# Optimization experiments

Hardware: AMD Instinct MI355X
Metric: run time of the kernel (lower is better)

Reference implementation:

```python
import jax, jax.numpy as jnp
import numpy as np

K = 2  # max_diffusion_step
UNITS = 128
NUM_NODES = 1024


def _diffusion_conv(x, support, W, b):
    # x: (B, N, D) ; Chebyshev diffusion over scaled Laplacian support (N, N)
    x0 = x
    x1 = jnp.einsum('nm,bmd->bnd', support, x0)
    xs = [x0, x1]
    for _ in range(K - 1):
        xs.append(2.0 * jnp.einsum('nm,bmd->bnd', support, xs[-1]) - xs[-2])
    feats = jnp.concatenate(xs, axis=-1)  # (B, N, D*(K+1))
    return feats @ W + b


def _gclstm_cell(x, h, c, support, W, b):
    gates = _diffusion_conv(jnp.concatenate([x, h], axis=-1), support, W, b)
    i, f, o, g = jnp.split(gates, 4, axis=-1)
    c_new = jax.nn.sigmoid(f) * c + jax.nn.sigmoid(i) * jnp.tanh(g)
    h_new = jax.nn.sigmoid(o) * jnp.tanh(c_new)
    return h_new, c_new


def setup_inputs() -> dict:
    key = jax.random.key(0)
    ks = jax.random.split(key, 8)
    B, S, N, H = 64, 12, NUM_NODES, UNITS

    # build scaled-Laplacian support from a sparse random symmetric adjacency
    rng = np.random.default_rng(0)
    A = (rng.random((N, N)) < 0.01).astype(np.float32)
    A = np.maximum(A, A.T)
    np.fill_diagonal(A, 0.0)
    d = A.sum(axis=1)
    d_is = 1.0 / np.sqrt(np.maximum(d, 1.0))
    L = np.eye(N, dtype=np.float32) - (d_is[:, None] * A * d_is[None, :])
    support = (L - np.eye(N, dtype=np.float32)).astype(np.float32)  # lambda_max ~ 2

    def lin(k, shape, fan_in):
        return jax.random.normal(k, shape, jnp.float32) / np.sqrt(fan_in)

    return {
        'inputs': jax.random.normal(ks[0], (B, N, 1), jnp.float32),
        'encoder_outputs': jax.random.normal(ks[1], (S, B, N, H), jnp.float32),
        'hidden_state': jax.random.normal(ks[2], (2, B, N, H), jnp.float32),
        'cell_state': jax.random.normal(ks[3], (2, B, N, H), jnp.float32),
        'supports': jnp.asarray(support),
        'w0': lin(ks[4], ((1 + H) * (K + 1), 4 * H), (1 + H) * (K + 1)),
        'b0': jnp.zeros((4 * H,), jnp.float32),
        'w1': lin(ks[5], ((H + H) * (K + 1), 4 * H), 2 * H * (K + 1)),
        'b1': jnp.zeros((4 * H,), jnp.float32),
        'attn_w': lin(ks[6], (H, H), H),
        'attn_b': jnp.zeros((H,), jnp.float32),
        'proj_w': lin(ks[7], (2 * H, 1), 2 * H),
        'proj_b': jnp.zeros((1,), jnp.float32),
    }


def reference(inputs, encoder_outputs, hidden_state, cell_state, supports,
              w0, b0, w1, b1, attn_w, attn_b, proj_w, proj_b):
    out = inputs
    hs, cs = [], []
    for layer, (W, b) in enumerate([(w0, b0), (w1, b1)]):
        h_new, c_new = _gclstm_cell(out, hidden_state[layer], cell_state[layer],
                                    supports, W, b)
        hs.append(h_new)
        cs.append(c_new)
        out = h_new  # (B, N, H)

    # additive attention: energy (S,B,N) -> softmax over S
    energy = jnp.tanh(encoder_outputs @ attn_w + attn_b)          # (S,B,N,H)
    energy = jnp.sum(energy * out[None], axis=-1)                 # (S,B,N)
    attention_weights = jax.nn.softmax(jnp.transpose(energy, (1, 2, 0)), axis=-1)  # (B,N,S)

    # bmm context gather
    context = jnp.einsum('bns,sbnh->bnh', attention_weights, encoder_outputs)

    cat = jnp.concatenate([out, context], axis=-1)                # (B,N,2H)
    projected = cat @ proj_w + proj_b                             # (B,N,out_dim)
    B = out.shape[0]
    output = projected.reshape(B, -1)                             # (B, N*out_dim)
    return output, jnp.stack(hs), jnp.stack(cs), attention_weights
```

## Files before the change

kernel.cpp:

```cpp
#include <hip/hip_runtime.h>
#include <hip/hip_bf16.h>
#include <stdint.h>

#define NB 64
#define NN 1024
#define NH 128
#define NS 12
#define BN (NB*NN)
#define D0 129
#define K0P 416
#define K1 768
#define NG 512
#define MAXNNZ 128
#define CH 16384
#define NCHUNK (BN/CH)

typedef __hip_bfloat16 bf16;
typedef float v4f __attribute__((ext_vector_type(4)));
typedef __bf16 v8bf __attribute__((ext_vector_type(8)));

__device__ __forceinline__ float bf2f(bf16 x) { return __bfloat162float(x); }
__device__ __forceinline__ bf16 f2bf(float x) { return __float2bfloat16(x); }
__device__ __forceinline__ float sane(float x) { return __builtin_isfinite(x) ? x : 0.f; }

__device__ __forceinline__ float loadF(const void* p, size_t i, int f32) {
  return f32 ? ((const float*)p)[i] : bf2f(((const bf16*)p)[i]);
}
__device__ __forceinline__ void storeF(void* p, size_t i, float v, int f32) {
  if (f32) ((float*)p)[i] = v; else ((bf16*)p)[i] = f2bf(v);
}
__device__ __forceinline__ v8bf load8(const void* p, size_t i, int f32) {
  v8bf r;
  if (f32) {
    const float* fp = (const float*)p + i;
#pragma unroll
    for (int j = 0; j < 8; ++j) r[j] = (__bf16)fp[j];
  } else {
    r = *(const v8bf*)((const bf16*)p + i);
  }
  return r;
}

__global__ void detect_dtype(const unsigned short* __restrict__ probe, int* __restrict__ flag) {
  int t = threadIdx.x;
  unsigned short x = probe[2 * t];
  int e = (x >> 7) & 0xFF;
  int insane = !((x & 0x7FFF) == 0 || (e >= 117 && e <= 131));
  __shared__ int cnt;
  if (t == 0) cnt = 0;
  __syncthreads();
  atomicAdd(&cnt, insane);
  __syncthreads();
  if (t == 0) *flag = (cnt > 64) ? 1 : 0;
}

__global__ void build_csr(const void* __restrict__ sup, int* __restrict__ cols,
                          float* __restrict__ vals, int* __restrict__ cnt,
                          const int* __restrict__ flag) {
  int f32 = *flag;
  int n = blockIdx.x;
  __shared__ int cn;
  if (threadIdx.x == 0) cn = 0;
  __syncthreads();
  for (int m = threadIdx.x; m < NN; m += blockDim.x) {
    float v = loadF(sup, (size_t)n * NN + m, f32);
    if (v != 0.0f && __builtin_isfinite(v)) {
      int slot = atomicAdd(&cn, 1);
      if (slot < MAXNNZ) { cols[n * MAXNNZ + slot] = m; vals[n * MAXNNZ + slot] = v; }
    }
  }
  __syncthreads();
  if (threadIdx.x == 0) cnt[n] = (cn < MAXNNZ) ? cn : MAXNNZ;
}

__global__ void pack_wt(const void* __restrict__ w, bf16* __restrict__ bt,
                        int K, int Kp, int Nn, const int* __restrict__ flag) {
  int f32 = *flag;
  int n = blockIdx.x;
  for (int k = threadIdx.x; k < Kp; k += blockDim.x) {
    float v = (k < K) ? loadF(w, (size_t)k * Nn + n, f32) : 0.0f;
    bt[(size_t)n * Kp + k] = f2bf(v);
  }
}

__global__ void diffuse0_a(const void* __restrict__ xin, const void* __restrict__ h0,
                           const int* __restrict__ cols, const float* __restrict__ vals,
                           const int* __restrict__ cnt, bf16* __restrict__ feats,
                           const int* __restrict__ flag, int R) {
  int f32 = *flag;
  int bn = R + blockIdx.x;
  int lbn = blockIdx.x;
  int n = bn & (NN - 1);
  int b = bn >> 10;
  int d = threadIdx.x;
  bf16* frow = feats + (size_t)lbn * K0P;
  if (d < D0) {
    float x0 = (d == 0) ? loadF(xin, bn, f32) : loadF(h0, (size_t)bn * NH + d - 1, f32);
    frow[d] = f2bf(x0);
    float acc = 0.f;
    int c = cnt[n];
    for (int j = 0; j < c; ++j) {
      int m = cols[n * MAXNNZ + j];
      float s = vals[n * MAXNNZ + j];
      int bm = (b << 10) | m;
      float xv = (d == 0) ? loadF(xin, bm, f32) : loadF(h0, (size_t)bm * NH + d - 1, f32);
      acc += s * xv;
    }
    frow[D0 + d] = f2bf(acc);
  } else if (d < D0 + (K0P - 3 * D0)) {
    frow[3 * D0 + (d - D0)] = f2bf(0.f);
  }
}

__global__ void diffuse0_b(const void* __restrict__ xin, const void* __restrict__ h0,
                           const int* __restrict__ cols, const float* __restrict__ vals,
                           const int* __restrict__ cnt, bf16* __restrict__ feats,
                           const int* __restrict__ flag, int R) {
  int f32 = *flag;
  int bn = R + blockIdx.x;
  int lbn = blockIdx.x;
  int n = bn & (NN - 1);
  int b = bn >> 10;
  int d = threadIdx.x;
  if (d >= D0) return;
  float x0 = (d == 0) ? loadF(xin, bn, f32) : loadF(h0, (size_t)bn * NH + d - 1, f32);
  float acc = -x0;
  int c = cnt[n];
  for (int j = 0; j < c; ++j) {
    int m = cols[n * MAXNNZ + j];
    float s = vals[n * MAXNNZ + j];
    int lbm = ((b << 10) | m) - R;
    float x1 = bf2f(feats[(size_t)lbm * K0P + D0 + d]);
    acc += 2.f * s * x1;
  }
  feats[(size_t)lbn * K0P + 2 * D0 + d] = f2bf(acc);
}

__global__ void diffuse1_a(const void* __restrict__ dout, size_t offH0,
                           const void* __restrict__ hidden, size_t offH1in,
                           const int* __restrict__ cols, const float* __restrict__ vals,
                           const int* __restrict__ cnt, bf16* __restrict__ feats,
                           const int* __restrict__ flag, int R) {
  int f32 = *flag;
  int bn = R + blockIdx.x;
  int lbn = blockIdx.x;
  int n = bn & (NN - 1);
  int b = bn >> 10;
  int d = threadIdx.x;
  bf16* frow = feats + (size_t)lbn * K1;
  float x0 = (d < NH) ? loadF(dout, offH0 + (size_t)bn * NH + d, f32)
                      : loadF(hidden, offH1in + (size_t)bn * NH + d - NH, f32);
  frow[d] = f2bf(x0);
  float acc = 0.f;
  int c = cnt[n];
  for (int j = 0; j < c; ++j) {
    int m = cols[n * MAXNNZ + j];
    float s = vals[n * MAXNNZ + j];
    size_t bm = (size_t)((b << 10) | m) * NH;
    float xv = (d < NH) ? loadF(dout, offH0 + bm + d, f32)
                        : loadF(hidden, offH1in + bm + d - NH, f32);
    acc += s * xv;
  }
  frow[256 + d] = f2bf(acc);
}

__global__ void diffuse1_b(const void* __restrict__ dout, size_t offH0,
                           const void* __restrict__ hidden, size_t offH1in,
                           const int* __restrict__ cols, const float* __restrict__ vals,
                           const int* __restrict__ cnt, bf16* __restrict__ feats,
                           const int* __restrict__ flag, int R) {
  int f32 = *flag;
  int bn = R + blockIdx.x;
  int lbn = blockIdx.x;
  int n = bn & (NN - 1);
  int b = bn >> 10;
  int d = threadIdx.x;
  float x0 = (d < NH) ? loadF(dout, offH0 + (size_t)bn * NH + d, f32)
                      : loadF(hidden, offH1in + (size_t)bn * NH + d - NH, f32);
  float acc = -x0;
  int c = cnt[n];
  for (int j = 0; j < c; ++j) {
    int m = cols[n * MAXNNZ + j];
    float s = vals[n * MAXNNZ + j];
    int lbm = ((b << 10) | m) - R;
    float x1 = bf2f(feats[(size_t)lbm * K1 + 256 + d]);
    acc += 2.f * s * x1;
  }
  feats[(size_t)lbn * K1 + 512 + d] = f2bf(acc);
}

__global__ __launch_bounds__(256) void gemm_bt(const bf16* __restrict__ A,
    const bf16* __restrict__ Bt, const void* __restrict__ bias,
    bf16* __restrict__ C, int Kd, const int* __restrict__ flag) {
  int f32 = *flag;
  __shared__ __align__(16) unsigned short As[128 * 32];
  __shared__ __align__(16) unsigned short Bs[128 * 32];
  const int tid = threadIdx.x;
  const int l = tid & 63;
  const int w = tid >> 6;
  const int wm = w >> 1, wn = w & 1;
  const int m0 = blockIdx.x * 128;
  const int n0 = blockIdx.y * 128;
  const bf16* Ab = A + (size_t)m0 * Kd;
  const bf16* Bb = Bt + (size_t)n0 * Kd;
  const int lr = l & 15, q = l >> 4;
  v4f acc[4][4] = {};
  for (int k0 = 0; k0 < Kd; k0 += 32) {
    v8bf ga[2], gb[2];
#pragma unroll
    for (int t = 0; t < 2; ++t) {
      int s = tid + 256 * t;
      int row = s >> 2, col = (s & 3) * 8;
      ga[t] = *(const v8bf*)(Ab + (size_t)row * Kd + k0 + col);
      gb[t] = *(const v8bf*)(Bb + (size_t)row * Kd + k0 + col);
    }
    __syncthreads();
#pragma unroll
    for (int t = 0; t < 2; ++t) {
      int s = tid + 256 * t;
      int row = s >> 2, col = (s & 3) * 8;
      *(v8bf*)&As[row * 32 + col] = ga[t];
      *(v8bf*)&Bs[row * 32 + col] = gb[t];
    }
    __syncthreads();
    v8bf af[4], bfv[4];
#pragma unroll
    for (int i = 0; i < 4; ++i) {
      af[i]  = *(const v8bf*)&As[(wm * 64 + i * 16 + lr) * 32 + q * 8];
      bfv[i] = *(const v8bf*)&Bs[(wn * 64 + i * 16 + lr) * 32 + q * 8];
    }
#pragma unroll
    for (int mt = 0; mt < 4; ++mt)
#pragma unroll
      for (int nt = 0; nt < 4; ++nt)
        acc[mt][nt] = __builtin_amdgcn_mfma_f32_16x16x32_bf16(af[mt], bfv[nt], acc[mt][nt], 0, 0, 0);
    __syncthreads();
  }
#pragma unroll
  for (int nt = 0; nt < 4; ++nt) {
    int n = n0 + wn * 64 + nt * 16 + lr;
    float bv = loadF(bias, n, f32);
#pragma unroll
    for (int mt = 0; mt < 4; ++mt)
#pragma unroll
      for (int r = 0; r < 4; ++r) {
        int m = m0 + wm * 64 + mt * 16 + q * 4 + r;
        C[(size_t)m * NG + n] = f2bf(acc[mt][nt][r] + bv);
      }
  }
}

__global__ __launch_bounds__(256) void gemm_energy(const void* __restrict__ enc,
    const bf16* __restrict__ Bt, const void* __restrict__ bias,
    const void* __restrict__ dout, size_t offH1, float* __restrict__ energy,
    const int* __restrict__ flag) {
  int f32 = *flag;
  __shared__ __align__(16) unsigned short As[128 * 32];
  __shared__ __align__(16) unsigned short Bs[128 * 32];
  const int tid = threadIdx.x;
  const int l = tid & 63;
  const int w = tid >> 6;
  const int wm = w >> 1, wn = w & 1;
  const int m0 = blockIdx.x * 128;
  const int lr = l & 15, q = l >> 4;
  v4f acc[4][4] = {};
  for (int k0 = 0; k0 < NH; k0 += 32) {
    v8bf ga[2], gb[2];
#pragma unroll
    for (int t = 0; t < 2; ++t) {
      int s = tid + 256 * t;
      int row = s >> 2, col = (s & 3) * 8;
      ga[t] = load8(enc, (size_t)(m0 + row) * NH + k0 + col, f32);
      gb[t] = *(const v8bf*)(Bt + (size_t)row * NH + k0 + col);
    }
    __syncthreads();
#pragma unroll
    for (int t = 0; t < 2; ++t) {
      int s = tid + 256 * t;
      int row = s >> 2, col = (s & 3) * 8;
      *(v8bf*)&As[row * 32 + col] = ga[t];
      *(v8bf*)&Bs[row * 32 + col] = gb[t];
    }
    __syncthreads();
    v8bf af[4], bfv[4];
#pragma unroll
    for (int i = 0; i < 4; ++i) {
      af[i]  = *(const v8bf*)&As[(wm * 64 + i * 16 + lr) * 32 + q * 8];
      bfv[i] = *(const v8bf*)&Bs[(wn * 64 + i * 16 + lr) * 32 + q * 8];
    }
#pragma unroll
    for (int mt = 0; mt < 4; ++mt)
#pragma unroll
      for (int nt = 0; nt < 4; ++nt)
        acc[mt][nt] = __builtin_amdgcn_mfma_f32_16x16x32_bf16(af[mt], bfv[nt], acc[mt][nt], 0, 0, 0);
    __syncthreads();
  }
#pragma unroll
  for (int mt = 0; mt < 4; ++mt) {
    float parts[4] = {0.f, 0.f, 0.f, 0.f};
#pragma unroll
    for (int nt = 0; nt < 4; ++nt) {
      int n = wn * 64 + nt * 16 + lr;
      float bv = loadF(bias, n, f32);
#pragma unroll
      for (int r = 0; r < 4; ++r) {
        int m = m0 + wm * 64 + mt * 16 + q * 4 + r;
        int bn = m & (BN - 1);
        float t = tanhf(acc[mt][nt][r] + bv);
        parts[r] += t * loadF(dout, offH1 + (size_t)bn * NH + n, f32);
      }
    }
#pragma unroll
    for (int r = 0; r < 4; ++r) {
      float v = parts[r];
      v += __shfl_xor(v, 1);
      v += __shfl_xor(v, 2);
      v += __shfl_xor(v, 4);
      v += __shfl_xor(v, 8);
      if (lr == 0) {
        int m = m0 + wm * 64 + mt * 16 + q * 4 + r;
        atomicAdd(&energy[m], sane(v));
      }
    }
  }
}

__global__ __launch_bounds__(128) void lstm_cell(const bf16* __restrict__ gates,
    const void* __restrict__ cell, size_t offCin, void* __restrict__ dout,
    size_t offH, size_t offC, const int* __restrict__ flag, int R) {
  int f32 = *flag;
  size_t lbn = blockIdx.x;
  size_t bn = (size_t)R + lbn;
  int h = threadIdx.x;
  const bf16* g = gates + lbn * NG;
  float iv = sane(bf2f(g[h]));
  float fv = sane(bf2f(g[NH + h]));
  float ov = sane(bf2f(g[2 * NH + h]));
  float gv = sane(bf2f(g[3 * NH + h]));
  float c = sane(loadF(cell, offCin + bn * NH + h, f32));
  float si = 1.f / (1.f + expf(-iv));
  float sf = 1.f / (1.f + expf(-fv));
  float so = 1.f / (1.f + expf(-ov));
  float cn = sf * c + si * tanhf(gv);
  float hn = so * tanhf(cn);
  storeF(dout, offC + bn * NH + h, cn, f32);
  storeF(dout, offH + bn * NH + h, hn, f32);
}

__global__ void softmax_s(const float* __restrict__ energy, float* __restrict__ attnf,
                          void* __restrict__ dout, size_t offAttn,
                          const int* __restrict__ flag) {
  int f32 = *flag;
  int bn = blockIdx.x * blockDim.x + threadIdx.x;
  float e[NS];
  float mx = -3.4e38f;
#pragma unroll
  for (int s = 0; s < NS; ++s) { e[s] = sane(energy[s * BN + bn]); mx = fmaxf(mx, e[s]); }
  float sum = 0.f;
#pragma unroll
  for (int s = 0; s < NS; ++s) { e[s] = expf(e[s] - mx); sum += e[s]; }
  float inv = 1.f / sum;
#pragma unroll
  for (int s = 0; s < NS; ++s) {
    float wv = e[s] * inv;
    attnf[(size_t)bn * NS + s] = wv;
    storeF(dout, offAttn + (size_t)bn * NS + s, wv, f32);
  }
}

__global__ __launch_bounds__(128) void context_proj(const void* __restrict__ enc,
    const float* __restrict__ attnf, void* __restrict__ dout, size_t offH1,
    const void* __restrict__ proj_w, const void* __restrict__ proj_b,
    const int* __restrict__ flag) {
  int f32 = *flag;
  int bn = blockIdx.x;
  int h = threadIdx.x;
  float ctx = 0.f;
#pragma unroll
  for (int s = 0; s < NS; ++s) {
    float aw = attnf[(size_t)bn * NS + s];
    ctx += aw * loadF(enc, ((size_t)s * BN + bn) * NH + h, f32);
  }
  float ov = loadF(dout, offH1 + (size_t)bn * NH + h, f32);
  float part = sane(ov * loadF(proj_w, h, f32) + ctx * loadF(proj_w, NH + h, f32));
#pragma unroll
  for (int mask = 1; mask < 64; mask <<= 1) part += __shfl_xor(part, mask);
  __shared__ float red[2];
  if ((h & 63) == 0) red[h >> 6] = part;
  __syncthreads();
  if (h == 0) storeF(dout, bn, red[0] + red[1] + loadF(proj_b, 0, f32), f32);
}

extern "C" void kernel_launch(void* const* d_in, const int* in_sizes, int n_in,
                              void* d_out, int out_size, void* d_ws, size_t ws_size,
                              hipStream_t stream) {
  const void* xin    = d_in[0];
  const void* enc    = d_in[1];
  const void* hidden = d_in[2];
  const void* cell   = d_in[3];
  const void* sup    = d_in[4];
  const void* w0     = d_in[5];
  const void* b0     = d_in[6];
  const void* w1     = d_in[7];
  const void* b1     = d_in[8];
  const void* aw     = d_in[9];
  const void* ab     = d_in[10];
  const void* pw     = d_in[11];
  const void* pb     = d_in[12];

  char* ws = (char*)d_ws;
  size_t off = 0;
  auto alloc = [&](size_t bytes) -> char* {
    char* p = ws + off;
    off += (bytes + 255) & ~(size_t)255;
    return p;
  };
  bf16*  feats    = (bf16*)alloc((size_t)CH * K1 * 2);
  bf16*  gates    = (bf16*)alloc((size_t)CH * NG * 2);
  float* energy   = (float*)alloc((size_t)NS * BN * 4);
  float* attnf    = (float*)alloc((size_t)BN * NS * 4);
  bf16*  Bt0      = (bf16*)alloc((size_t)NG * K0P * 2);
  bf16*  Bt1      = (bf16*)alloc((size_t)NG * K1 * 2);
  bf16*  BtA      = (bf16*)alloc((size_t)NH * NH * 2);
  int*   csr_cols = (int*)alloc((size_t)NN * MAXNNZ * 4);
  float* csr_vals = (float*)alloc((size_t)NN * MAXNNZ * 4);
  int*   csr_cnt  = (int*)alloc((size_t)NN * 4);
  int*   flag     = (int*)alloc(256);

  const size_t OFF_HS   = (size_t)BN;
  const size_t OFF_CS   = OFF_HS + (size_t)2 * BN * NH;
  const size_t OFF_ATTN = OFF_CS + (size_t)2 * BN * NH;
  const size_t OFF_H0 = OFF_HS;
  const size_t OFF_H1 = OFF_HS + (size_t)BN * NH;
  const size_t OFF_C0 = OFF_CS;
  const size_t OFF_C1 = OFF_CS + (size_t)BN * NH;
  const size_t LAYER1 = (size_t)BN * NH;

  detect_dtype<<<1, 256, 0, stream>>>((const unsigned short*)cell, flag);
  build_csr<<<NN, 256, 0, stream>>>(sup, csr_cols, csr_vals, csr_cnt, flag);
  pack_wt<<<NG, 256, 0, stream>>>(w0, Bt0, 387, K0P, NG, flag);
  pack_wt<<<NG, 256, 0, stream>>>(w1, Bt1, K1, K1, NG, flag);
  pack_wt<<<NH, 128, 0, stream>>>(aw, BtA, NH, NH, NH, flag);
  hipMemsetAsync(energy, 0, (size_t)NS * BN * 4, stream);

  for (int c = 0; c < NCHUNK; ++c) {
    int R = c * CH;
    diffuse0_a<<<CH, 192, 0, stream>>>(xin, hidden, csr_cols, csr_vals, csr_cnt, feats, flag, R);
    diffuse0_b<<<CH, 192, 0, stream>>>(xin, hidden, csr_cols, csr_vals, csr_cnt, feats, flag, R);
    dim3 g(CH / 128, NG / 128);
    gemm_bt<<<g, 256, 0, stream>>>(feats, Bt0, b0, gates, K0P, flag);
    lstm_cell<<<CH, 128, 0, stream>>>(gates, cell, 0, d_out, OFF_H0, OFF_C0, flag, R);
  }

  for (int c = 0; c < NCHUNK; ++c) {
    int R = c * CH;
    diffuse1_a<<<CH, 256, 0, stream>>>(d_out, OFF_H0, hidden, LAYER1,
                                       csr_cols, csr_vals, csr_cnt, feats, flag, R);
    diffuse1_b<<<CH, 256, 0, stream>>>(d_out, OFF_H0, hidden, LAYER1,
                                       csr_cols, csr_vals, csr_cnt, feats, flag, R);
    dim3 g(CH / 128, NG / 128);
    gemm_bt<<<g, 256, 0, stream>>>(feats, Bt1, b1, gates, K1, flag);
    lstm_cell<<<CH, 128, 0, stream>>>(gates, cell, LAYER1, d_out, OFF_H1, OFF_C1, flag, R);
  }

  gemm_energy<<<NS * BN / 128, 256, 0, stream>>>(enc, BtA, ab, d_out, OFF_H1, energy, flag);
  softmax_s<<<BN / 256, 256, 0, stream>>>(energy, attnf, d_out, OFF_ATTN, flag);
  context_proj<<<BN, 128, 0, stream>>>(enc, attnf, d_out, OFF_H1, pw, pb, flag);
}
```

Measured before the change: 2.098 ms.

## Preload attention weights to LDS, replace atomics, use fast math, vectorize fp32 loads

The energy GEMM now loads the whole 128x128 attention weight into padded shared memory once per block. The two column-half partial sums are reduced in shared memory and written directly, replacing global atomics and the memset that zeroed them. Sigmoid, tanh and softmax exp switch to __expf-based fast approximations, the fp32 path of load8 uses float4 vector loads, and context_proj handles two rows per 256-thread block. Together these reduce global traffic, atomics and transcendental cost, at the price of slightly lower math accuracy and more LDS per block.

```diff
diff --git a/kernel.cpp b/kernel.cpp
--- a/kernel.cpp
+++ b/kernel.cpp
@@ -22,6 +22,8 @@
 __device__ __forceinline__ float bf2f(bf16 x) { return __bfloat162float(x); }
 __device__ __forceinline__ bf16 f2bf(float x) { return __float2bfloat16(x); }
 __device__ __forceinline__ float sane(float x) { return __builtin_isfinite(x) ? x : 0.f; }
+__device__ __forceinline__ float sigf(float x) { return 1.f / (1.f + __expf(-x)); }
+__device__ __forceinline__ float tanhfast(float x) { return 1.f - 2.f / (1.f + __expf(2.f * x)); }
 
 __device__ __forceinline__ float loadF(const void* p, size_t i, int f32) {
   return f32 ? ((const float*)p)[i] : bf2f(((const bf16*)p)[i]);
@@ -30,15 +32,17 @@
   if (f32) ((float*)p)[i] = v; else ((bf16*)p)[i] = f2bf(v);
 }
 __device__ __forceinline__ v8bf load8(const void* p, size_t i, int f32) {
-  v8bf r;
   if (f32) {
-    const float* fp = (const float*)p + i;
-#pragma unroll
-    for (int j = 0; j < 8; ++j) r[j] = (__bf16)fp[j];
-  } else {
-    r = *(const v8bf*)((const bf16*)p + i);
-  }
-  return r;
+    const float4 a = *(const float4*)((const float*)p + i);
+    const float4 b = *(const float4*)((const float*)p + i + 4);
+    union { v8bf v; __hip_bfloat162 h[4]; } u;
+    u.h[0] = __float22bfloat162_rn(make_float2(a.x, a.y));
+    u.h[1] = __float22bfloat162_rn(make_float2(a.z, a.w));
+    u.h[2] = __float22bfloat162_rn(make_float2(b.x, b.y));
+    u.h[3] = __float22bfloat162_rn(make_float2(b.z, b.w));
+    return u.v;
+  }
+  return *(const v8bf*)((const bf16*)p + i);
 }
 
 __global__ void detect_dtype(const unsigned short* __restrict__ probe, int* __restrict__ flag) {
@@ -250,28 +254,36 @@
   }
 }
 
+#define BPAD 136
 __global__ __launch_bounds__(256) void gemm_energy(const void* __restrict__ enc,
     const bf16* __restrict__ Bt, const void* __restrict__ bias,
     const void* __restrict__ dout, size_t offH1, float* __restrict__ energy,
     const int* __restrict__ flag) {
   int f32 = *flag;
   __shared__ __align__(16) unsigned short As[128 * 32];
-  __shared__ __align__(16) unsigned short Bs[128 * 32];
+  __shared__ __align__(16) unsigned short Bsf[128 * BPAD];
+  __shared__ float ered[2][128];
   const int tid = threadIdx.x;
   const int l = tid & 63;
   const int w = tid >> 6;
   const int wm = w >> 1, wn = w & 1;
   const int m0 = blockIdx.x * 128;
   const int lr = l & 15, q = l >> 4;
+
+#pragma unroll
+  for (int i = tid; i < 2048; i += 256) {
+    int row = i >> 4, chunk = i & 15;
+    *(v8bf*)&Bsf[row * BPAD + chunk * 8] = *(const v8bf*)(Bt + (size_t)row * NH + chunk * 8);
+  }
+
   v4f acc[4][4] = {};
   for (int k0 = 0; k0 < NH; k0 += 32) {
-    v8bf ga[2], gb[2];
+    v8bf ga[2];
 #pragma unroll
     for (int t = 0; t < 2; ++t) {
       int s = tid + 256 * t;
       int row = s >> 2, col = (s & 3) * 8;
       ga[t] = load8(enc, (size_t)(m0 + row) * NH + k0 + col, f32);
-      gb[t] = *(const v8bf*)(Bt + (size_t)row * NH + k0 + col);
     }
     __syncthreads();
 #pragma unroll
@@ -279,14 +291,13 @@
       int s = tid + 256 * t;
       int row = s >> 2, col = (s & 3) * 8;
       *(v8bf*)&As[row * 32 + col] = ga[t];
-      *(v8bf*)&Bs[row * 32 + col] = gb[t];
     }
     __syncthreads();
     v8bf af[4], bfv[4];
 #pragma unroll
     for (int i = 0; i < 4; ++i) {
       af[i]  = *(const v8bf*)&As[(wm * 64 + i * 16 + lr) * 32 + q * 8];
-      bfv[i] = *(const v8bf*)&Bs[(wn * 64 + i * 16 + lr) * 32 + q * 8];
+      bfv[i] = *(const v8bf*)&Bsf[(wn * 64 + i * 16 + lr) * BPAD + k0 + q * 8];
     }
 #pragma unroll
     for (int mt = 0; mt < 4; ++mt)
@@ -306,7 +317,7 @@
       for (int r = 0; r < 4; ++r) {
         int m = m0 + wm * 64 + mt * 16 + q * 4 + r;
         int bn = m & (BN - 1);
-        float t = tanhf(acc[mt][nt][r] + bv);
+        float t = tanhfast(acc[mt][nt][r] + bv);
         parts[r] += t * loadF(dout, offH1 + (size_t)bn * NH + n, f32);
       }
     }
@@ -318,11 +329,13 @@
       v += __shfl_xor(v, 4);
       v += __shfl_xor(v, 8);
       if (lr == 0) {
-        int m = m0 + wm * 64 + mt * 16 + q * 4 + r;
-        atomicAdd(&energy[m], sane(v));
+        int lm = wm * 64 + mt * 16 + q * 4 + r;
+        ered[wn][lm] = v;
       }
     }
   }
+  __syncthreads();
+  if (tid < 128) energy[m0 + tid] = sane(ered[0][tid] + ered[1][tid]);
 }
 
 __global__ __launch_bounds__(128) void lstm_cell(const bf16* __restrict__ gates,
@@ -338,11 +351,8 @@
   float ov = sane(bf2f(g[2 * NH + h]));
   float gv = sane(bf2f(g[3 * NH + h]));
   float c = sane(loadF(cell, offCin + bn * NH + h, f32));
-  float si = 1.f / (1.f + expf(-iv));
-  float sf = 1.f / (1.f + expf(-fv));
-  float so = 1.f / (1.f + expf(-ov));
-  float cn = sf * c + si * tanhf(gv);
-  float hn = so * tanhf(cn);
+  float cn = sigf(fv) * c + sigf(iv) * tanhfast(gv);
+  float hn = sigf(ov) * tanhfast(cn);
   storeF(dout, offC + bn * NH + h, cn, f32);
   storeF(dout, offH + bn * NH + h, hn, f32);
 }
@@ -358,7 +368,7 @@
   for (int s = 0; s < NS; ++s) { e[s] = sane(energy[s * BN + bn]); mx = fmaxf(mx, e[s]); }
   float sum = 0.f;
 #pragma unroll
-  for (int s = 0; s < NS; ++s) { e[s] = expf(e[s] - mx); sum += e[s]; }
+  for (int s = 0; s < NS; ++s) { e[s] = __expf(e[s] - mx); sum += e[s]; }
   float inv = 1.f / sum;
 #pragma unroll
   for (int s = 0; s < NS; ++s) {
@@ -368,13 +378,14 @@
   }
 }
 
-__global__ __launch_bounds__(128) void context_proj(const void* __restrict__ enc,
+__global__ __launch_bounds__(256) void context_proj(const void* __restrict__ enc,
     const float* __restrict__ attnf, void* __restrict__ dout, size_t offH1,
     const void* __restrict__ proj_w, const void* __restrict__ proj_b,
     const int* __restrict__ flag) {
   int f32 = *flag;
-  int bn = blockIdx.x;
-  int h = threadIdx.x;
+  int sub = threadIdx.x >> 7;
+  int h = threadIdx.x & 127;
+  int bn = blockIdx.x * 2 + sub;
   float ctx = 0.f;
 #pragma unroll
   for (int s = 0; s < NS; ++s) {
@@ -385,10 +396,10 @@
   float part = sane(ov * loadF(proj_w, h, f32) + ctx * loadF(proj_w, NH + h, f32));
 #pragma unroll
   for (int mask = 1; mask < 64; mask <<= 1) part += __shfl_xor(part, mask);
-  __shared__ float red[2];
-  if ((h & 63) == 0) red[h >> 6] = part;
-  __syncthreads();
-  if (h == 0) storeF(dout, bn, red[0] + red[1] + loadF(proj_b, 0, f32), f32);
+  __shared__ float red[4];
+  if ((threadIdx.x & 63) == 0) red[threadIdx.x >> 6] = part;
+  __syncthreads();
+  if (h == 0) storeF(dout, bn, red[sub * 2] + red[sub * 2 + 1] + loadF(proj_b, 0, f32), f32);
 }
 
 extern "C" void kernel_launch(void* const* d_in, const int* in_sizes, int n_in,
@@ -441,7 +452,6 @@
   pack_wt<<<NG, 256, 0, stream>>>(w0, Bt0, 387, K0P, NG, flag);
   pack_wt<<<NG, 256, 0, stream>>>(w1, Bt1, K1, K1, NG, flag);
   pack_wt<<<NH, 128, 0, stream>>>(aw, BtA, NH, NH, NH, flag);
-  hipMemsetAsync(energy, 0, (size_t)NS * BN * 4, stream);
 
   for (int c = 0; c < NCHUNK; ++c) {
     int R = c * CH;
@@ -465,5 +475,5 @@
 
   gemm_energy<<<NS * BN / 128, 256, 0, stream>>>(enc, BtA, ab, d_out, OFF_H1, energy, flag);
   softmax_s<<<BN / 256, 256, 0, stream>>>(energy, attnf, d_out, OFF_ATTN, flag);
-  context_proj<<<BN, 128, 0, stream>>>(enc, attnf, d_out, OFF_H1, pw, pb, flag);
-}
+  context_proj<<<BN / 2, 256, 0, stream>>>(enc, attnf, d_out, OFF_H1, pw, pb, flag);
+}
```

After: 1.974 ms. 1.06x faster.
